# Performance work log

Measured on AMD Instinct MI355X. Metric: run time of the kernel, lower is better.

Reference implementation:

```python
import jax, jax.numpy as jnp
import numpy as np


def _conv_relu(x, w, b):
    # keras Conv2D: NHWC input, HWIO kernel, VALID padding, stride 1, relu
    y = jax.lax.conv_general_dilated(
        x, w, window_strides=(1, 1), padding='VALID',
        dimension_numbers=('NHWC', 'HWIO', 'NHWC'))
    return jax.nn.relu(y + b)


def _maxpool2(x):
    # keras MaxPooling2D((2,2)): window 2x2, stride 2, VALID
    return jax.lax.reduce_window(
        x, -jnp.inf, jax.lax.max,
        window_dimensions=(1, 2, 2, 1), window_strides=(1, 2, 2, 1),
        padding='VALID')


def setup_inputs() -> dict:
    key = jax.random.key(0)
    ks = jax.random.split(key, 8)
    B = 4096
    return {
        'x': jax.random.normal(ks[0], (B, 14, 14, 1), jnp.float32),
        'conv1_w': jax.random.normal(ks[1], (3, 3, 1, 32), jnp.float32) * 0.1,
        'conv1_b': jnp.zeros((32,), jnp.float32),
        'conv2_w': jax.random.normal(ks[2], (3, 3, 32, 64), jnp.float32) * 0.05,
        'conv2_b': jnp.zeros((64,), jnp.float32),
        # trainable grid, initialized as tf.linspace(0,1,grid_size=50)
        'grid': jnp.linspace(0.0, 1.0, 50, dtype=jnp.float32),
        # KANLayer splines: output_dim=128 weights, each (input_dim=256, grid_size=50)
        'kan1_w': jax.random.normal(ks[3], (128, 256, 50), jnp.float32) * 0.05,
        # SimplifiedKANLayer splines: output_dim=64 weights, each (input_dim=128,)
        'kan2_w': jax.random.normal(ks[4], (64, 128), jnp.float32) * 0.05,
        'dense_w': jax.random.normal(ks[5], (64, 10), jnp.float32) * 0.05,
        'dense_b': jnp.zeros((10,), jnp.float32),
    }


def reference(x, conv1_w, conv1_b, conv2_w, conv2_b, grid, kan1_w, kan2_w,
              dense_w, dense_b):
    h = _conv_relu(x, conv1_w, conv1_b)   # (B,12,12,32)
    h = _maxpool2(h)                      # (B,6,6,32)
    h = _conv_relu(h, conv2_w, conv2_b)   # (B,4,4,64)
    h = _maxpool2(h)                      # (B,2,2,64)
    B = h.shape[0]
    h = h.reshape(B, -1)                  # (B,256) keras Flatten order (H,W,C)
    # KANLayer: linear hat basis relu(1-|x-g|) per (feature,grid), contracted
    # against per-output coefficients: out[b,o] = sum_{d,g} W[o,d,g]*basis[b,d,g]
    basis = jax.nn.relu(1.0 - jnp.abs(h[:, :, None] - grid[None, None, :]))  # (B,256,50)
    h = jnp.einsum('bdg,odg->bo', basis, kan1_w)  # (B,128)
    # SimplifiedKANLayer: out[b,o] = sum_d W2[o,d]*relu(h[b,d])
    h = jnp.einsum('bd,od->bo', jax.nn.relu(h), kan2_w)  # (B,64)
    return jax.nn.softmax(h @ dense_w + dense_b, axis=-1)  # (B,10)
```

## Files before the change

### kernel.cpp

```cpp
#include <hip/hip_runtime.h>
#include <hip/hip_bf16.h>
#include <hip/hip_fp16.h>

typedef _Float16 f16x8 __attribute__((ext_vector_type(8)));
typedef float f32x4 __attribute__((ext_vector_type(4)));

#define NBC 8
#define TBLB 256

__global__ __launch_bounds__(256) void k_front(
    const float* __restrict__ x, const float* __restrict__ w1,
    const float* __restrict__ b1, const float* __restrict__ w2,
    const float* __restrict__ b2, const float* __restrict__ kan1_w,
    float* __restrict__ h2, __half* __restrict__ tabN) {
  __shared__ float xs[NBC * 224];
  __shared__ float w1s[288];
  __shared__ float b1s[32];
  __shared__ _Float16 w2l[18432];
  __shared__ _Float16 h1l[NBC * 36 * 40];
  int t = threadIdx.x;
  int bid = blockIdx.x;

  if (bid < TBLB) {
    if (t < 128) {
      int d = bid, o = t;
      const float* wp = kan1_w + (size_t)o * 12800 + (size_t)d * 50;
      float w[50];
#pragma unroll
      for (int i = 0; i < 25; ++i) {
        float2 v = *(const float2*)(wp + 2 * i);
        w[2 * i] = v.x;
        w[2 * i + 1] = v.y;
      }
      float lowW = w[0], lowG = 0.f;
      float highW = 0.f, highG = 0.f;
#pragma unroll
      for (int g = 1; g < 50; ++g) {
        highW += w[g];
        highG += w[g] * ((float)g * (1.0f / 49.0f));
      }
      __half* trow = tabN + (size_t)d * 197 * 128 + o;
      const float inv98 = 1.0f / 98.0f;
#pragma unroll
      for (int j = 0; j < 98; ++j) {
        float A = highW - lowW;
        float Bc = (lowW + highW) + lowG - highG;
        float c0 = (float)(2 * j) * inv98 + 0.5f * inv98;
        float c1 = c0 + inv98;
        trow[(size_t)(2 * j) * 128] = __float2half(fmaf(A, c0, Bc));
        trow[(size_t)(2 * j + 1) * 128] = __float2half(fmaf(A, c1, Bc));
        if (j + 1 <= 49) {
          float wg = w[j + 1], gg = (float)(j + 1) * (1.0f / 49.0f);
          lowW += wg; lowG += wg * gg;
          highW -= wg; highG -= wg * gg;
        }
        if (j >= 48) {
          float wg = w[j - 48], gg = (float)(j - 48) * (1.0f / 49.0f);
          lowW -= wg; lowG -= wg * gg;
        }
      }
      trow[(size_t)196 * 128] = __float2half(0.f);
    }
    return;
  }

  int cb = bid - TBLB;
  int b0 = cb * NBC;
  {
    for (int i = t; i < NBC * 224; i += 256) {
      int blb = i / 224;
      int rem = i - blb * 224;
      int r = rem >> 4;
      int cc = rem & 15;
      xs[i] = (cc < 14) ? x[(size_t)(b0 + blb) * 196 + r * 14 + cc] : 0.f;
    }
    for (int i = t; i < 288; i += 256) w1s[i] = w1[i];
    if (t < 32) b1s[t] = b1[t];
    for (int r = t; r < 18432; r += 256) {
      int n = r & 63;
      int row = r >> 6;
      int ci = row & 31;
      int tap = row >> 5;
      w2l[((tap * 4 + (ci >> 3)) * 64 + n) * 8 + (ci & 7)] = (_Float16)w2[r];
    }
  }
  __syncthreads();
  int p = t >> 6;
  int c = t & 63;
  {
    int ch = c & 31;
    int half = c >> 5;
    float wr[9];
#pragma unroll
    for (int j = 0; j < 9; ++j) wr[j] = w1s[j * 32 + ch];
    float bias = b1s[ch];
    int y0 = 3 * half;
#pragma unroll
    for (int bl2 = 0; bl2 < 2; ++bl2) {
      const float* xb = xs + (2 * p + bl2) * 224;
      _Float16* hrow = h1l + (2 * p + bl2) * 1440 + ch;
#pragma unroll
      for (int yy = 0; yy < 3; ++yy) {
        int y = y0 + yy;
        float xr[4][16];
#pragma unroll
        for (int r = 0; r < 4; ++r) {
          float4* dstp = (float4*)xr[r];
          const float4* srcp = (const float4*)(xb + (2 * y + r) * 16);
#pragma unroll
          for (int q = 0; q < 4; ++q) dstp[q] = srcp[q];
        }
#pragma unroll
        for (int xx = 0; xx < 6; ++xx) {
          float m = -1e30f;
#pragma unroll
          for (int py = 0; py < 2; ++py)
#pragma unroll
            for (int px = 0; px < 2; ++px) {
              float s = 0.f;
#pragma unroll
              for (int dy = 0; dy < 3; ++dy)
#pragma unroll
                for (int dx = 0; dx < 3; ++dx)
                  s = fmaf(xr[py + dy][2 * xx + px + dx], wr[dy * 3 + dx], s);
              m = fmaxf(m, s);
            }
          hrow[(y * 6 + xx) * 40] = (_Float16)fmaxf(m + bias, 0.f);
        }
      }
    }
  }
  __syncthreads();
  {
    int lm = t & 15;
    int lk = (t >> 4) & 3;
    int mbase = (lm >> 2) * 6 + (lm & 3);
    f32x4 acc[2][4];
#pragma unroll
    for (int j = 0; j < 2; ++j)
#pragma unroll
      for (int nt = 0; nt < 4; ++nt) acc[j][nt] = (f32x4){0.f, 0.f, 0.f, 0.f};
    const _Float16* h0 = &h1l[(2 * p) * 1440 + lk * 8];
    const _Float16* h1p = h0 + 1440;
#pragma unroll
    for (int tap = 0; tap < 9; ++tap) {
      int tapoff = (tap / 3) * 6 + (tap % 3);
      int po = (mbase + tapoff) * 40;
      f16x8 a0 = *(const f16x8*)(h0 + po);
      f16x8 a1 = *(const f16x8*)(h1p + po);
      const _Float16* wb = &w2l[((tap * 4 + lk) * 64 + lm) * 8];
      f16x8 bf0 = *(const f16x8*)(wb);
      f16x8 bf1 = *(const f16x8*)(wb + 128);
      f16x8 bf2 = *(const f16x8*)(wb + 256);
      f16x8 bf3 = *(const f16x8*)(wb + 384);
      acc[0][0] = __builtin_amdgcn_mfma_f32_16x16x32_f16(a0, bf0, acc[0][0], 0, 0, 0);
      acc[0][1] = __builtin_amdgcn_mfma_f32_16x16x32_f16(a0, bf1, acc[0][1], 0, 0, 0);
      acc[0][2] = __builtin_amdgcn_mfma_f32_16x16x32_f16(a0, bf2, acc[0][2], 0, 0, 0);
      acc[0][3] = __builtin_amdgcn_mfma_f32_16x16x32_f16(a0, bf3, acc[0][3], 0, 0, 0);
      acc[1][0] = __builtin_amdgcn_mfma_f32_16x16x32_f16(a1, bf0, acc[1][0], 0, 0, 0);
      acc[1][1] = __builtin_amdgcn_mfma_f32_16x16x32_f16(a1, bf1, acc[1][1], 0, 0, 0);
      acc[1][2] = __builtin_amdgcn_mfma_f32_16x16x32_f16(a1, bf2, acc[1][2], 0, 0, 0);
      acc[1][3] = __builtin_amdgcn_mfma_f32_16x16x32_f16(a1, bf3, acc[1][3], 0, 0, 0);
    }
    float bias[4];
#pragma unroll
    for (int nt = 0; nt < 4; ++nt) bias[nt] = b2[nt * 16 + lm];
#pragma unroll
    for (int j = 0; j < 2; ++j) {
      float* outb = h2 + (size_t)(b0 + 2 * p + j) * 256;
#pragma unroll
      for (int nt = 0; nt < 4; ++nt) {
        f32x4 A = acc[j][nt];
        float m01 = fmaxf(A.x, A.y);
        float m23 = fmaxf(A.z, A.w);
        m01 = fmaxf(m01, __shfl_xor(m01, 16));
        m23 = fmaxf(m23, __shfl_xor(m23, 16));
        float val = (lk & 1) ? m23 : m01;
        outb[lk * 64 + nt * 16 + lm] = fmaxf(val + bias[nt], 0.f);
      }
    }
  }
}

#define KB 4
__global__ __launch_bounds__(256) void k_back(
    const float* __restrict__ h2, const __half* __restrict__ tabN,
    const float* __restrict__ kan2_w, const float* __restrict__ dense_w,
    const float* __restrict__ dense_b, float* __restrict__ out) {
  __shared__ unsigned short meta[256 * KB];
  __shared__ float wl[64 * 132];
  __shared__ float vs[KB][128];
  __shared__ float us[KB][64];
  __shared__ float dl[640];
  __shared__ float ls[KB][10];
  int t = threadIdx.x;
  int b0 = blockIdx.x * KB;
  for (int i = t; i < 256 * KB; i += 256) {
    int b = i >> 8;
    int d = i & 255;
    float h = h2[(size_t)(b0 + b) * 256 + d];
    int k = (int)(h * 98.0f);
    k = k < 0 ? 0 : (k > 196 ? 196 : k);
    meta[d * KB + b] = (unsigned short)(d * 197 + k);
  }
  for (int i = t; i < 2048; i += 256) {
    float4 v = ((const float4*)kan2_w)[i];
    int o = i >> 5;
    int dcol = (i & 31) * 4;
    *(float4*)&wl[o * 132 + dcol] = v;
  }
  for (int i = t; i < 640; i += 256) dl[i] = dense_w[i];
  __syncthreads();
  {
    int w = t >> 6;
    int l = t & 63;
    int lq = l >> 4;
    int lo = l & 15;
    int phase0 = blockIdx.x & 3;
    float acc[8];
#pragma unroll
    for (int e = 0; e < 8; ++e) acc[e] = 0.f;
#pragma unroll
    for (int ph = 0; ph < 4; ++ph) {
      int d0 = ((phase0 + ph) & 3) << 6;
#pragma unroll 4
      for (int dq = 0; dq < 16; ++dq) {
        int dd = d0 + 4 * dq + lq;
        int off = ((int)meta[dd * KB + w]) << 7;
        float4 raw = *(const float4*)(tabN + off + lo * 8);
        __half2 p0 = __builtin_bit_cast(__half2, raw.x);
        __half2 p1 = __builtin_bit_cast(__half2, raw.y);
        __half2 p2 = __builtin_bit_cast(__half2, raw.z);
        __half2 p3 = __builtin_bit_cast(__half2, raw.w);
        float2 f0 = __half22float2(p0);
        float2 f1 = __half22float2(p1);
        float2 f2 = __half22float2(p2);
        float2 f3 = __half22float2(p3);
        acc[0] += f0.x; acc[1] += f0.y;
        acc[2] += f1.x; acc[3] += f1.y;
        acc[4] += f2.x; acc[5] += f2.y;
        acc[6] += f3.x; acc[7] += f3.y;
      }
    }
#pragma unroll
    for (int e = 0; e < 8; ++e) {
      acc[e] += __shfl_xor(acc[e], 16);
      acc[e] += __shfl_xor(acc[e], 32);
    }
    if (lq == 0) {
      float* vp = &vs[w][lo * 8];
      *(float4*)vp = make_float4(fmaxf(acc[0], 0.f), fmaxf(acc[1], 0.f),
                                 fmaxf(acc[2], 0.f), fmaxf(acc[3], 0.f));
      *(float4*)(vp + 4) = make_float4(fmaxf(acc[4], 0.f), fmaxf(acc[5], 0.f),
                                       fmaxf(acc[6], 0.f), fmaxf(acc[7], 0.f));
    }
  }
  __syncthreads();
  {
    int w = t >> 6;
    int o = t & 63;
    float a = 0.f;
    const float* wrow = &wl[o * 132];
    const float* v0 = &vs[w][0];
#pragma unroll
    for (int d4 = 0; d4 < 128; d4 += 4) {
      float4 wq = *(const float4*)(wrow + d4);
      float4 q0 = *(const float4*)(v0 + d4);
      a = fmaf(wq.x, q0.x, a); a = fmaf(wq.y, q0.y, a);
      a = fmaf(wq.z, q0.z, a); a = fmaf(wq.w, q0.w, a);
    }
    us[w][o] = a;
  }
  __syncthreads();
  if (t < KB * 10) {
    int b = t / 10;
    int j = t - b * 10;
    float s = dense_b[j];
    for (int k2 = 0; k2 < 64; ++k2) s = fmaf(us[b][k2], dl[k2 * 10 + j], s);
    ls[b][j] = s;
  }
  __syncthreads();
  if (t < KB) {
    int b = t;
    float m = -1e30f;
#pragma unroll
    for (int j = 0; j < 10; ++j) m = fmaxf(m, ls[b][j]);
    float e[10];
    float sum = 0.f;
#pragma unroll
    for (int j = 0; j < 10; ++j) {
      e[j] = __expf(ls[b][j] - m);
      sum += e[j];
    }
    float inv = 1.0f / sum;
#pragma unroll
    for (int j = 0; j < 10; ++j) out[(size_t)(b0 + b) * 10 + j] = e[j] * inv;
  }
}

extern "C" void kernel_launch(void* const* d_in, const int* in_sizes, int n_in,
                              void* d_out, int out_size, void* d_ws, size_t ws_size,
                              hipStream_t stream) {
  const float* x      = (const float*)d_in[0];
  const float* w1     = (const float*)d_in[1];
  const float* b1     = (const float*)d_in[2];
  const float* w2     = (const float*)d_in[3];
  const float* b2     = (const float*)d_in[4];
  const float* kan1_w = (const float*)d_in[6];
  const float* kan2_w = (const float*)d_in[7];
  const float* dw     = (const float*)d_in[8];
  const float* db     = (const float*)d_in[9];
  float* out = (float*)d_out;
  int B = in_sizes[0] / 196;

  char* wsb = (char*)d_ws;
  float* h2 = (float*)wsb;
  size_t off1 = (size_t)B * 256 * sizeof(float);
  __half* tabN = (__half*)(wsb + off1);

  k_front<<<dim3(TBLB + B / NBC), dim3(256), 0, stream>>>(
      x, w1, b1, w2, b2, kan1_w, h2, tabN);
  k_back<<<dim3(B / KB), dim3(256), 0, stream>>>(
      h2, tabN, kan2_w, dw, db, out);
}
```

Before: 118.7 us.

## Halve front batch per block, pack KAN2 weights as half2, vectorize back accumulators

Measured after the change: 114.6 us. 1.04x faster.

```diff
diff --git a/kernel.cpp b/kernel.cpp
--- a/kernel.cpp
+++ b/kernel.cpp
@@ -2,10 +2,11 @@
 #include <hip/hip_bf16.h>
 #include <hip/hip_fp16.h>
 
+typedef float v2f __attribute__((ext_vector_type(2)));
 typedef _Float16 f16x8 __attribute__((ext_vector_type(8)));
 typedef float f32x4 __attribute__((ext_vector_type(4)));
 
-#define NBC 8
+#define NBC 4
 #define TBLB 256
 
 __global__ __launch_bounds__(256) void k_front(
@@ -95,89 +96,75 @@
     for (int j = 0; j < 9; ++j) wr[j] = w1s[j * 32 + ch];
     float bias = b1s[ch];
     int y0 = 3 * half;
-#pragma unroll
-    for (int bl2 = 0; bl2 < 2; ++bl2) {
-      const float* xb = xs + (2 * p + bl2) * 224;
-      _Float16* hrow = h1l + (2 * p + bl2) * 1440 + ch;
-#pragma unroll
-      for (int yy = 0; yy < 3; ++yy) {
-        int y = y0 + yy;
-        float xr[4][16];
-#pragma unroll
-        for (int r = 0; r < 4; ++r) {
-          float4* dstp = (float4*)xr[r];
-          const float4* srcp = (const float4*)(xb + (2 * y + r) * 16);
-#pragma unroll
-          for (int q = 0; q < 4; ++q) dstp[q] = srcp[q];
-        }
-#pragma unroll
-        for (int xx = 0; xx < 6; ++xx) {
-          float m = -1e30f;
-#pragma unroll
-          for (int py = 0; py < 2; ++py)
-#pragma unroll
-            for (int px = 0; px < 2; ++px) {
-              float s = 0.f;
-#pragma unroll
-              for (int dy = 0; dy < 3; ++dy)
-#pragma unroll
-                for (int dx = 0; dx < 3; ++dx)
-                  s = fmaf(xr[py + dy][2 * xx + px + dx], wr[dy * 3 + dx], s);
-              m = fmaxf(m, s);
-            }
-          hrow[(y * 6 + xx) * 40] = (_Float16)fmaxf(m + bias, 0.f);
-        }
-      }
-    }
-  }
-  __syncthreads();
-  {
-    int lm = t & 15;
-    int lk = (t >> 4) & 3;
+    const float* xb = xs + p * 224;
+    _Float16* hrow = h1l + p * 1440 + ch;
+#pragma unroll
+    for (int yy = 0; yy < 3; ++yy) {
+      int y = y0 + yy;
+      float xr[4][16];
+#pragma unroll
+      for (int r = 0; r < 4; ++r) {
+        float4* dstp = (float4*)xr[r];
+        const float4* srcp = (const float4*)(xb + (2 * y + r) * 16);
+#pragma unroll
+        for (int q = 0; q < 4; ++q) dstp[q] = srcp[q];
+      }
+#pragma unroll
+      for (int xx = 0; xx < 6; ++xx) {
+        float m = -1e30f;
+#pragma unroll
+        for (int py = 0; py < 2; ++py)
+#pragma unroll
+          for (int px = 0; px < 2; ++px) {
+            float s = 0.f;
+#pragma unroll
+            for (int dy = 0; dy < 3; ++dy)
+#pragma unroll
+              for (int dx = 0; dx < 3; ++dx)
+                s = fmaf(xr[py + dy][2 * xx + px + dx], wr[dy * 3 + dx], s);
+            m = fmaxf(m, s);
+          }
+        hrow[(y * 6 + xx) * 40] = (_Float16)fmaxf(m + bias, 0.f);
+      }
+    }
+  }
+  __syncthreads();
+  {
+    int lm = c & 15;
+    int lk = c >> 4;
     int mbase = (lm >> 2) * 6 + (lm & 3);
-    f32x4 acc[2][4];
-#pragma unroll
-    for (int j = 0; j < 2; ++j)
-#pragma unroll
-      for (int nt = 0; nt < 4; ++nt) acc[j][nt] = (f32x4){0.f, 0.f, 0.f, 0.f};
-    const _Float16* h0 = &h1l[(2 * p) * 1440 + lk * 8];
-    const _Float16* h1p = h0 + 1440;
+    f32x4 acc[4];
+#pragma unroll
+    for (int nt = 0; nt < 4; ++nt) acc[nt] = (f32x4){0.f, 0.f, 0.f, 0.f};
+    const _Float16* h0 = &h1l[p * 1440 + lk * 8];
 #pragma unroll
     for (int tap = 0; tap < 9; ++tap) {
       int tapoff = (tap / 3) * 6 + (tap % 3);
       int po = (mbase + tapoff) * 40;
       f16x8 a0 = *(const f16x8*)(h0 + po);
-      f16x8 a1 = *(const f16x8*)(h1p + po);
       const _Float16* wb = &w2l[((tap * 4 + lk) * 64 + lm) * 8];
       f16x8 bf0 = *(const f16x8*)(wb);
       f16x8 bf1 = *(const f16x8*)(wb + 128);
       f16x8 bf2 = *(const f16x8*)(wb + 256);
       f16x8 bf3 = *(const f16x8*)(wb + 384);
-      acc[0][0] = __builtin_amdgcn_mfma_f32_16x16x32_f16(a0, bf0, acc[0][0], 0, 0, 0);
-      acc[0][1] = __builtin_amdgcn_mfma_f32_16x16x32_f16(a0, bf1, acc[0][1], 0, 0, 0);
-      acc[0][2] = __builtin_amdgcn_mfma_f32_16x16x32_f16(a0, bf2, acc[0][2], 0, 0, 0);
-      acc[0][3] = __builtin_amdgcn_mfma_f32_16x16x32_f16(a0, bf3, acc[0][3], 0, 0, 0);
-      acc[1][0] = __builtin_amdgcn_mfma_f32_16x16x32_f16(a1, bf0, acc[1][0], 0, 0, 0);
-      acc[1][1] = __builtin_amdgcn_mfma_f32_16x16x32_f16(a1, bf1, acc[1][1], 0, 0, 0);
-      acc[1][2] = __builtin_amdgcn_mfma_f32_16x16x32_f16(a1, bf2, acc[1][2], 0, 0, 0);
-      acc[1][3] = __builtin_amdgcn_mfma_f32_16x16x32_f16(a1, bf3, acc[1][3], 0, 0, 0);
+      acc[0] = __builtin_amdgcn_mfma_f32_16x16x32_f16(a0, bf0, acc[0], 0, 0, 0);
+      acc[1] = __builtin_amdgcn_mfma_f32_16x16x32_f16(a0, bf1, acc[1], 0, 0, 0);
+      acc[2] = __builtin_amdgcn_mfma_f32_16x16x32_f16(a0, bf2, acc[2], 0, 0, 0);
+      acc[3] = __builtin_amdgcn_mfma_f32_16x16x32_f16(a0, bf3, acc[3], 0, 0, 0);
     }
     float bias[4];
 #pragma unroll
     for (int nt = 0; nt < 4; ++nt) bias[nt] = b2[nt * 16 + lm];
-#pragma unroll
-    for (int j = 0; j < 2; ++j) {
-      float* outb = h2 + (size_t)(b0 + 2 * p + j) * 256;
-#pragma unroll
-      for (int nt = 0; nt < 4; ++nt) {
-        f32x4 A = acc[j][nt];
-        float m01 = fmaxf(A.x, A.y);
-        float m23 = fmaxf(A.z, A.w);
-        m01 = fmaxf(m01, __shfl_xor(m01, 16));
-        m23 = fmaxf(m23, __shfl_xor(m23, 16));
-        float val = (lk & 1) ? m23 : m01;
-        outb[lk * 64 + nt * 16 + lm] = fmaxf(val + bias[nt], 0.f);
-      }
+    float* outb = h2 + (size_t)(b0 + p) * 256;
+#pragma unroll
+    for (int nt = 0; nt < 4; ++nt) {
+      f32x4 A = acc[nt];
+      float m01 = fmaxf(A.x, A.y);
+      float m23 = fmaxf(A.z, A.w);
+      m01 = fmaxf(m01, __shfl_xor(m01, 16));
+      m23 = fmaxf(m23, __shfl_xor(m23, 16));
+      float val = (lk & 1) ? m23 : m01;
+      outb[lk * 64 + nt * 16 + lm] = fmaxf(val + bias[nt], 0.f);
     }
   }
 }
@@ -188,7 +175,7 @@
     const float* __restrict__ kan2_w, const float* __restrict__ dense_w,
     const float* __restrict__ dense_b, float* __restrict__ out) {
   __shared__ unsigned short meta[256 * KB];
-  __shared__ float wl[64 * 132];
+  __shared__ __half2 wl2[64 * 64];
   __shared__ float vs[KB][128];
   __shared__ float us[KB][64];
   __shared__ float dl[640];
@@ -206,8 +193,10 @@
   for (int i = t; i < 2048; i += 256) {
     float4 v = ((const float4*)kan2_w)[i];
     int o = i >> 5;
-    int dcol = (i & 31) * 4;
-    *(float4*)&wl[o * 132 + dcol] = v;
+    int dp0 = (i & 31) * 2;
+    wl2[dp0 * 64 + (o ^ (dp0 & 31))] = __floats2half2_rn(v.x, v.y);
+    int dp1 = dp0 + 1;
+    wl2[dp1 * 64 + (o ^ (dp1 & 31))] = __floats2half2_rn(v.z, v.w);
   }
   for (int i = t; i < 640; i += 256) dl[i] = dense_w[i];
   __syncthreads();
@@ -216,43 +205,42 @@
     int l = t & 63;
     int lq = l >> 4;
     int lo = l & 15;
-    int phase0 = blockIdx.x & 3;
-    float acc[8];
-#pragma unroll
-    for (int e = 0; e < 8; ++e) acc[e] = 0.f;
-#pragma unroll
-    for (int ph = 0; ph < 4; ++ph) {
-      int d0 = ((phase0 + ph) & 3) << 6;
+    int phase0 = blockIdx.x & 7;
+    v2f acc[4];
+#pragma unroll
+    for (int e = 0; e < 4; ++e) acc[e] = (v2f){0.f, 0.f};
+#pragma unroll
+    for (int ph = 0; ph < 8; ++ph) {
+      int d0 = ((phase0 + ph) & 7) << 5;
 #pragma unroll 4
-      for (int dq = 0; dq < 16; ++dq) {
+      for (int dq = 0; dq < 8; ++dq) {
         int dd = d0 + 4 * dq + lq;
         int off = ((int)meta[dd * KB + w]) << 7;
         float4 raw = *(const float4*)(tabN + off + lo * 8);
-        __half2 p0 = __builtin_bit_cast(__half2, raw.x);
-        __half2 p1 = __builtin_bit_cast(__half2, raw.y);
-        __half2 p2 = __builtin_bit_cast(__half2, raw.z);
-        __half2 p3 = __builtin_bit_cast(__half2, raw.w);
-        float2 f0 = __half22float2(p0);
-        float2 f1 = __half22float2(p1);
-        float2 f2 = __half22float2(p2);
-        float2 f3 = __half22float2(p3);
-        acc[0] += f0.x; acc[1] += f0.y;
-        acc[2] += f1.x; acc[3] += f1.y;
-        acc[4] += f2.x; acc[5] += f2.y;
-        acc[6] += f3.x; acc[7] += f3.y;
-      }
-    }
-#pragma unroll
-    for (int e = 0; e < 8; ++e) {
-      acc[e] += __shfl_xor(acc[e], 16);
-      acc[e] += __shfl_xor(acc[e], 32);
+        float2 f0 = __half22float2(__builtin_bit_cast(__half2, raw.x));
+        float2 f1 = __half22float2(__builtin_bit_cast(__half2, raw.y));
+        float2 f2 = __half22float2(__builtin_bit_cast(__half2, raw.z));
+        float2 f3 = __half22float2(__builtin_bit_cast(__half2, raw.w));
+        acc[0] += (v2f){f0.x, f0.y};
+        acc[1] += (v2f){f1.x, f1.y};
+        acc[2] += (v2f){f2.x, f2.y};
+        acc[3] += (v2f){f3.x, f3.y};
+      }
+    }
+#pragma unroll
+    for (int e = 0; e < 4; ++e) {
+      acc[e].x += __shfl_xor(acc[e].x, 16);
+      acc[e].y += __shfl_xor(acc[e].y, 16);
+      acc[e].x += __shfl_xor(acc[e].x, 32);
+      acc[e].y += __shfl_xor(acc[e].y, 32);
     }
     if (lq == 0) {
       float* vp = &vs[w][lo * 8];
-      *(float4*)vp = make_float4(fmaxf(acc[0], 0.f), fmaxf(acc[1], 0.f),
-                                 fmaxf(acc[2], 0.f), fmaxf(acc[3], 0.f));
-      *(float4*)(vp + 4) = make_float4(fmaxf(acc[4], 0.f), fmaxf(acc[5], 0.f),
-                                       fmaxf(acc[6], 0.f), fmaxf(acc[7], 0.f));
+      *(float4*)vp = make_float4(fmaxf(acc[0].x, 0.f), fmaxf(acc[0].y, 0.f),
+                                 fmaxf(acc[1].x, 0.f), fmaxf(acc[1].y, 0.f));
+      *(float4*)(vp + 4) =
+          make_float4(fmaxf(acc[2].x, 0.f), fmaxf(acc[2].y, 0.f),
+                      fmaxf(acc[3].x, 0.f), fmaxf(acc[3].y, 0.f));
     }
   }
   __syncthreads();
@@ -260,14 +248,14 @@
     int w = t >> 6;
     int o = t & 63;
     float a = 0.f;
-    const float* wrow = &wl[o * 132];
     const float* v0 = &vs[w][0];
-#pragma unroll
-    for (int d4 = 0; d4 < 128; d4 += 4) {
-      float4 wq = *(const float4*)(wrow + d4);
-      float4 q0 = *(const float4*)(v0 + d4);
-      a = fmaf(wq.x, q0.x, a); a = fmaf(wq.y, q0.y, a);
-      a = fmaf(wq.z, q0.z, a); a = fmaf(wq.w, q0.w, a);
+#pragma unroll 8
+    for (int dp = 0; dp < 64; ++dp) {
+      __half2 wq = wl2[dp * 64 + (o ^ (dp & 31))];
+      float2 wf = __half22float2(wq);
+      float2 vq = *(const float2*)(v0 + 2 * dp);
+      a = fmaf(wf.x, vq.x, a);
+      a = fmaf(wf.y, vq.y, a);
     }
     us[w][o] = a;
   }
```
